# Optimization experiments

Hardware: AMD Instinct MI355X
Metric: run time of the kernel (lower is better)

## Reference

```python
import jax, jax.numpy as jnp
import numpy as np
from jax import lax

B, T, V, D, H, DH, L, INTER, K, OUT, MAXDUR, MAXLEN = 8, 128, 256, 384, 6, 64, 4, 1536, 3, 80, 8, 2048
TMEL = T * MAXDUR  # fixed padded mel length (max possible sum of durations)


def _pe(maxlen, d):
    # SinCosPositionalEncoding buffer, shape [maxlen, d]
    den = jnp.exp(-jnp.arange(0, d, 2).astype(jnp.float32) * (np.log(10000.0) / d))
    pos = jnp.arange(maxlen, dtype=jnp.float32)[:, None]
    pe = jnp.zeros((maxlen, d), jnp.float32)
    pe = pe.at[:, 0::2].set(jnp.sin(pos * den))
    pe = pe.at[:, 1::2].set(jnp.cos(pos * den))
    return pe


def _ln(x, g, b):
    m = jnp.mean(x, -1, keepdims=True)
    v = jnp.mean((x - m) ** 2, -1, keepdims=True)
    return (x - m) * lax.rsqrt(v + 1e-5) * g + b


def _conv1d(x, w, b):
    # x: [B,T,Cin], w: [K,Cin,Cout], SAME padding
    return lax.conv_general_dilated(x, w, (1,), 'SAME', dimension_numbers=('NWC', 'WIO', 'NWC')) + b


def _layer(x, mask_add, wq, wk, wv, wo, g1, b1, c1w, c1b, c2w, c2b, g2, b2):
    Bx, Tx, _ = x.shape
    q = (x @ wq).reshape(Bx, Tx, H, DH)
    k = (x @ wk).reshape(Bx, Tx, H, DH)
    v = (x @ wv).reshape(Bx, Tx, H, DH)
    s = jnp.einsum('bqhd,bkhd->bhqk', q, k) / jnp.sqrt(jnp.float32(DH))
    s = s + mask_add[:, None, None, :]  # additive -inf key mask
    a = jax.nn.softmax(s, axis=-1)
    o = jnp.einsum('bhqk,bkhd->bqhd', a, v).reshape(Bx, Tx, H * DH) @ wo
    x = _ln(x + o, g1, b1)
    h = jax.nn.relu(_conv1d(x, c1w, c1b))
    h = _conv1d(h, c2w, c2b)
    return _ln(x + h, g2, b2)


def _stack(x, mask_add, ps):
    for i in range(L):
        x = _layer(x, mask_add, *(p[i] for p in ps))
    return x


def _forward(tokens, token_lengths, durations,
             emb,
             enc_wq, enc_wk, enc_wv, enc_wo, enc_ln1g, enc_ln1b, enc_c1w, enc_c1b, enc_c2w, enc_c2b, enc_ln2g, enc_ln2b,
             dec_wq, dec_wk, dec_wv, dec_wo, dec_ln1g, dec_ln1b, dec_c1w, dec_c1b, dec_c2w, dec_c2b, dec_ln2g, dec_ln2b,
             dp_c1w, dp_c1b, dp_ln1g, dp_ln1b, dp_c2w, dp_c2b, dp_ln2g, dp_ln2b, dp_w, dp_b,
             out_w, out_b):
    x = emb[tokens]  # [B,T,D]
    pe = _pe(MAXLEN, D)
    # faithful to the torch code: pos_embedding is [maxlen,1,D] and indexed by dim-0 of a
    # batch-first tensor, so PE is indexed by BATCH index and broadcast over time; plus the
    # model adds `emb + (emb + pe)` -> 2*emb + pe.
    x = 2.0 * x + pe[:x.shape[0]][:, None, :]
    am = jnp.where(jnp.arange(T)[None, :] > token_lengths[:, None], -jnp.inf, 0.0)
    enc = _stack(x, am, (enc_wq, enc_wk, enc_wv, enc_wo, enc_ln1g, enc_ln1b,
                         enc_c1w, enc_c1b, enc_c2w, enc_c2b, enc_ln2g, enc_ln2b))
    # duration predictor: conv-relu-LN x2 + linear -> [B,T]
    h = _ln(jax.nn.relu(_conv1d(enc, dp_c1w, dp_c1b)), dp_ln1g, dp_ln1b)
    h = _ln(jax.nn.relu(_conv1d(h, dp_c2w, dp_c2b)), dp_ln2g, dp_ln2b)
    length_predictions = (h @ dp_w + dp_b)[..., 0]
    # length regulator (vectorized duplicate_by_duration, fixed TMEL padding)
    mel_len = jnp.sum(durations, axis=1)  # [B]
    cs = jnp.cumsum(durations, axis=1)    # [B,T]
    pos = jnp.arange(TMEL)
    lr = ((pos[None, None, :] < cs[:, :, None]) & (pos[None, None, :] >= (cs - durations)[:, :, None])).astype(enc.dtype)  # [B,T,TMEL]
    dec_in = jnp.einsum('btm,btd->bmd', lr, enc)  # [B,TMEL,D]
    keep = (pos[None, :] <= mel_len[:, None]).astype(dec_in.dtype)
    dec_in = dec_in * keep[:, :, None]
    am2 = jnp.where(pos[None, :] > mel_len[:, None], -jnp.inf, 0.0)
    dec = _stack(dec_in, am2, (dec_wq, dec_wk, dec_wv, dec_wo, dec_ln1g, dec_ln1b,
                               dec_c1w, dec_c1b, dec_c2w, dec_c2b, dec_ln2g, dec_ln2b))
    out = (dec @ out_w + out_b).transpose(0, 2, 1)  # [B,OUT,TMEL]
    return out, length_predictions


def setup_inputs() -> dict:
    key = jax.random.key(0)
    ks = jax.random.split(key, 64)
    cnt = [2]
    def nrm(shape):
        cnt[0] += 1
        return jax.random.normal(ks[cnt[0]], shape, jnp.float32) * 0.02
    inp = {}
    inp['tokens'] = jax.random.randint(ks[0], (B, T), 0, V)
    inp['token_lengths'] = jax.random.randint(ks[1], (B,), T // 2, T)
    inp['durations'] = jax.random.randint(ks[2], (B, T), 1, MAXDUR + 1)
    inp['emb'] = nrm((V, D))
    for pre in ('enc', 'dec'):
        inp[pre + '_wq'] = nrm((L, D, H * DH))
        inp[pre + '_wk'] = nrm((L, D, H * DH))
        inp[pre + '_wv'] = nrm((L, D, H * DH))
        inp[pre + '_wo'] = nrm((L, H * DH, D))
        inp[pre + '_ln1g'] = jnp.ones((L, D), jnp.float32)
        inp[pre + '_ln1b'] = jnp.zeros((L, D), jnp.float32)
        inp[pre + '_c1w'] = nrm((L, K, D, INTER))
        inp[pre + '_c1b'] = jnp.zeros((L, INTER), jnp.float32)
        inp[pre + '_c2w'] = nrm((L, K, INTER, D))
        inp[pre + '_c2b'] = jnp.zeros((L, D), jnp.float32)
        inp[pre + '_ln2g'] = jnp.ones((L, D), jnp.float32)
        inp[pre + '_ln2b'] = jnp.zeros((L, D), jnp.float32)
    inp['dp_c1w'] = nrm((K, D, D)); inp['dp_c1b'] = jnp.zeros((D,), jnp.float32)
    inp['dp_ln1g'] = jnp.ones((D,), jnp.float32); inp['dp_ln1b'] = jnp.zeros((D,), jnp.float32)
    inp['dp_c2w'] = nrm((K, D, D)); inp['dp_c2b'] = jnp.zeros((D,), jnp.float32)
    inp['dp_ln2g'] = jnp.ones((D,), jnp.float32); inp['dp_ln2b'] = jnp.zeros((D,), jnp.float32)
    inp['dp_w'] = nrm((D, 1)); inp['dp_b'] = jnp.zeros((1,), jnp.float32)
    inp['out_w'] = nrm((D, OUT)); inp['out_b'] = jnp.zeros((OUT,), jnp.float32)
    return inp


def reference(tokens, token_lengths, durations,
              emb,
              enc_wq, enc_wk, enc_wv, enc_wo, enc_ln1g, enc_ln1b, enc_c1w, enc_c1b, enc_c2w, enc_c2b, enc_ln2g, enc_ln2b,
              dec_wq, dec_wk, dec_wv, dec_wo, dec_ln1g, dec_ln1b, dec_c1w, dec_c1b, dec_c2w, dec_c2b, dec_ln2g, dec_ln2b,
              dp_c1w, dp_c1b, dp_ln1g, dp_ln1b, dp_c2w, dp_c2b, dp_ln2g, dp_ln2b, dp_w, dp_b,
              out_w, out_b):
    return _forward(tokens, token_lengths, durations, emb,
                    enc_wq, enc_wk, enc_wv, enc_wo, enc_ln1g, enc_ln1b, enc_c1w, enc_c1b, enc_c2w, enc_c2b, enc_ln2g, enc_ln2b,
                    dec_wq, dec_wk, dec_wv, dec_wo, dec_ln1g, dec_ln1b, dec_c1w, dec_c1b, dec_c2w, dec_c2b, dec_ln2g, dec_ln2b,
                    dp_c1w, dp_c1b, dp_ln1g, dp_ln1b, dp_c2w, dp_c2b, dp_ln2g, dp_ln2b, dp_w, dp_b,
                    out_w, out_b)
```

## Files before the change

kernel.cpp:

```cpp
#include <hip/hip_runtime.h>
#include <math.h>

typedef __bf16 bf16;
typedef __attribute__((ext_vector_type(8))) __bf16 bf16x8;
typedef __attribute__((ext_vector_type(4))) float f32x4;

constexpr int B_ = 8;
constexpr int T_ = 128;
constexpr int D_ = 384;
constexpr int H_ = 6;
constexpr int DH_ = 64;
constexpr int L_ = 4;
constexpr int INTER_ = 1536;
constexpr int OUT_C = 80;
constexpr int TMEL_ = 1024;
constexpr int HD_ = 384;
constexpr int QKV_N = 1152;

__device__ __forceinline__ int xcd_swizzle(int bid, int nwg) {
  if (nwg & 7) return bid;
  return (bid & 7) * (nwg >> 3) + (bid >> 3);
}

__global__ __launch_bounds__(256) void embed_kernel(
    const int* __restrict__ tokens, const float* __restrict__ emb,
    float* __restrict__ X, bf16* __restrict__ Xbf) {
  int i = blockIdx.x * 256 + threadIdx.x;
  if (i >= B_ * T_ * D_) return;
  int d = i % D_;
  int bt = i / D_;
  int b = bt / T_, t = bt % T_;
  int tok = tokens[bt];
  int i2 = d & ~1;
  const float c = 9.210340371976184f / (float)D_;
  float freq = expf(-(float)i2 * c);
  float ang = (float)b * freq;
  float pe = (d & 1) ? cosf(ang) : sinf(ang);
  float v = 2.0f * emb[(size_t)tok * D_ + d] + pe;
  X[i] = v;
  Xbf[((size_t)b * (T_ + 2) + 1 + t) * D_ + d] = (bf16)v;
}

__global__ void enc_mask_kernel(const int* __restrict__ tl, float* __restrict__ maske) {
  int i = blockIdx.x * 256 + threadIdx.x;
  if (i >= B_ * T_) return;
  int b = i / T_, t = i % T_;
  maske[i] = (t > tl[b]) ? -INFINITY : 0.0f;
}

__global__ __launch_bounds__(256) void transpose_w_kernel(
    const float* __restrict__ src, long srcLS, bf16* __restrict__ dst,
    long dstLS, int K, int N, int rowOfs) {
  src += (size_t)blockIdx.z * srcLS;
  dst += (size_t)blockIdx.z * dstLS;
  __shared__ float tile[32][33];
  const int tx = threadIdx.x & 31, ty = threadIdx.x >> 5;
  const int n0 = blockIdx.x * 32, k0 = blockIdx.y * 32;
#pragma unroll
  for (int j = 0; j < 4; ++j)
    tile[ty + j * 8][tx] =
        (n0 + tx < N) ? src[(size_t)(k0 + ty + j * 8) * N + n0 + tx] : 0.0f;
  __syncthreads();
#pragma unroll
  for (int j = 0; j < 4; ++j)
    dst[(size_t)(n0 + rowOfs + ty + j * 8) * K + k0 + tx] = (bf16)tile[tx][ty + j * 8];
}

__global__ void zero_pads3_kernel(bf16* a, bf16* c, bf16* m, int Tp) {
  int b = blockIdx.x >> 1, side = blockIdx.x & 1;
  size_t row = (size_t)b * (Tp + 2) + (side ? (Tp + 1) : 0);
  bf16* buf = (blockIdx.y == 0) ? a : (blockIdx.y == 1) ? c : m;
  int C = (blockIdx.y == 2) ? INTER_ : D_;
  for (int cc = threadIdx.x; cc < C; cc += 256) buf[row * C + cc] = (bf16)0.0f;
}

__global__ __launch_bounds__(256) void transpose_v_kernel(
    const bf16* __restrict__ QKV, bf16* __restrict__ VT,
    const int* __restrict__ lens, int T) {
  const int tb = blockIdx.x, db = blockIdx.y, bh = blockIdx.z;
  const int b = bh / H_, h = bh % H_;
  const int ntiles = min(T >> 6, (lens[b] + 64) >> 6);
  if (tb >= ntiles * 2) return;
  __shared__ float tile[32][33];
  const int tx = threadIdx.x & 31, ty = threadIdx.x >> 5;
  const size_t src = ((size_t)b * (T + 2) + 1 + tb * 32) * QKV_N + 768 + h * DH_ + db * 32;
#pragma unroll
  for (int j = 0; j < 4; ++j)
    tile[ty + 8 * j][tx] = (float)QKV[src + (size_t)(ty + 8 * j) * QKV_N + tx];
  __syncthreads();
  const size_t dst = ((size_t)(b * H_ + h) * DH_ + db * 32) * T + tb * 32;
#pragma unroll
  for (int j = 0; j < 4; ++j)
    VT[dst + (size_t)(ty + 8 * j) * T + tx] = (bf16)tile[tx][ty + 8 * j];
}

template <int TP>
__global__ __launch_bounds__(256) void mfma_gemm_kernel(
    const bf16* __restrict__ A, int lda, int aofs,
    const bf16* __restrict__ WT, int ldw, int kslice,
    const float* __restrict__ bias, int relu,
    float* __restrict__ Cf, float* __restrict__ Cf2,
    bf16* __restrict__ Cbf, int ldc, int transC,
    const int* __restrict__ nact) {
  __shared__ bf16 As[3][128 * 32];
  __shared__ bf16 Bs[3][128 * 32];
  const int tid = threadIdx.x;
  const int lane = tid & 63;
  const int wave = tid >> 6;
  const int wr = wave >> 1, wc = wave & 1;

  const int nT = gridDim.x, mT = gridDim.y;
  const int nwg = nT * mT * gridDim.z;
  int bid = blockIdx.x + nT * (blockIdx.y + mT * blockIdx.z);
  int wid = xcd_swizzle(bid, nwg);
  const int bx = wid % nT;
  int tmp = wid / nT;
  const int by = tmp % mT;
  const int z = tmp / mT;

  const int rowBase = by * 128;
  const int colBase = bx * 128;
  const int k0beg = z * kslice;
  const int nt = kslice / 32;
  const int bb = rowBase / TP;
  constexpr int LASTT = TP / 128 - 1;
  if (nact) {
    int tloc = (rowBase - bb * TP) >> 7;
    if (tloc >= nact[bb] && tloc != LASTT) return;
  }
  const long pr0 = (long)bb * (TP + 2) + 1 + (rowBase - bb * TP);
  const long abase = pr0 * (long)lda - aofs;

  const int srow = tid >> 2, scb = tid & 3;

  auto stage = [&](int t, int buf) {
    const int k0 = k0beg + t * 32;
#pragma unroll
    for (int e = 0; e < 2; ++e) {
      int idx = e * 256 + tid;
      int lrow = srow + e * 64;
      const bf16* gp = A + abase + (long)lrow * lda + k0 + ((scb ^ ((lrow >> 1) & 3)) << 3);
      __builtin_amdgcn_global_load_lds(
          (const __attribute__((address_space(1))) unsigned int*)gp,
          (__attribute__((address_space(3))) unsigned int*)(As[buf] + idx * 8), 16, 0, 0);
    }
#pragma unroll
    for (int e = 0; e < 2; ++e) {
      int idx = e * 256 + tid;
      int lrow = srow + e * 64;
      const bf16* gp = WT + (long)(colBase + lrow) * ldw + k0 + ((scb ^ ((lrow >> 1) & 3)) << 3);
      __builtin_amdgcn_global_load_lds(
          (const __attribute__((address_space(1))) unsigned int*)gp,
          (__attribute__((address_space(3))) unsigned int*)(Bs[buf] + idx * 8), 16, 0, 0);
    }
  };

  f32x4 acc[4][4] = {};
  const int g = lane >> 4, l15 = lane & 15;

  stage(0, 0);
  if (nt > 1) stage(1, 1);
  int cur = 0;
  for (int t = 0; t < nt; ++t) {
    if (t + 2 < nt) {
      int sb = cur + 2;
      if (sb >= 3) sb -= 3;
      stage(t + 2, sb);
    }
    int ahead = nt - 1 - t;
    if (ahead >= 2)
      asm volatile("s_waitcnt vmcnt(8)" ::: "memory");
    else if (ahead == 1)
      asm volatile("s_waitcnt vmcnt(4)" ::: "memory");
    else
      asm volatile("s_waitcnt vmcnt(0)" ::: "memory");
    __builtin_amdgcn_s_barrier();
    asm volatile("" ::: "memory");

    const bf16* Asb = As[cur];
    const bf16* Bsb = Bs[cur];
    bf16x8 af[4], bw[4];
#pragma unroll
    for (int m = 0; m < 4; ++m) {
      int row = wr * 64 + m * 16 + l15;
      int cb = g ^ ((row >> 1) & 3);
      af[m] = *(const bf16x8*)(Asb + row * 32 + cb * 8);
    }
#pragma unroll
    for (int n = 0; n < 4; ++n) {
      int row = wc * 64 + n * 16 + l15;
      int cb = g ^ ((row >> 1) & 3);
      bw[n] = *(const bf16x8*)(Bsb + row * 32 + cb * 8);
    }
#pragma unroll
    for (int m = 0; m < 4; ++m)
#pragma unroll
      for (int n = 0; n < 4; ++n)
        acc[m][n] = __builtin_amdgcn_mfma_f32_16x16x32_bf16(af[m], bw[n], acc[m][n], 0, 0, 0);

    asm volatile("" ::: "memory");
    __builtin_amdgcn_s_barrier();
    cur = (cur + 1 == 3) ? 0 : cur + 1;
  }

  float* Cfz = z ? Cf2 : Cf;
  const float* biasz = z ? nullptr : bias;
  const int qr = (lane >> 4) * 4;
  const int qc = lane & 15;
#pragma unroll
  for (int m = 0; m < 4; ++m) {
    int lrow = wr * 64 + m * 16 + qr;
#pragma unroll
    for (int n = 0; n < 4; ++n) {
      int gcol = colBase + wc * 64 + n * 16 + qc;
      float bv = (biasz && (!transC || gcol < OUT_C)) ? biasz[gcol] : 0.0f;
#pragma unroll
      for (int q = 0; q < 4; ++q) {
        float v = acc[m][n][q] + bv;
        if (relu) v = fmaxf(v, 0.0f);
        if (transC) {
          if (gcol < OUT_C)
            Cfz[((long)bb * OUT_C + gcol) * TMEL_ + (rowBase - bb * TP + lrow + q)] = v;
        } else {
          if (Cfz) Cfz[(long)(rowBase + lrow + q) * ldc + gcol] = v;
          if (Cbf) Cbf[(pr0 + lrow + q) * ldc + gcol] = (bf16)v;
        }
      }
    }
  }
}

__global__ __launch_bounds__(256) void attn4_kernel(
    const bf16* __restrict__ QKV, const bf16* __restrict__ VT,
    const float* __restrict__ maskadd, const int* __restrict__ lens,
    const int* __restrict__ nactp, bf16* __restrict__ Obf, int T) {
  const int nQT = gridDim.x;
  const int nwg = nQT * H_ * B_;
  int bid = blockIdx.x + nQT * (blockIdx.y + H_ * blockIdx.z);
  int wid = xcd_swizzle(bid, nwg);
  const int qt = wid % nQT;
  int tmp = wid / nQT;
  const int h = tmp % H_;
  const int b = tmp / H_;
  if (nactp) {
    int tloc = qt >> 1;
    if (tloc >= nactp[b] && tloc != ((T >> 7) - 1)) return;
  }

  const int tid = threadIdx.x;
  const int lane = tid & 63;
  const int wave = tid >> 6;
  const int l15 = lane & 15, g = lane >> 4;

  __shared__ bf16 Ks[64 * 64];
  __shared__ bf16 Vts[64 * 64];
  __shared__ bf16 Ps[4][16 * 64];
  __shared__ float mask_s[TMEL_];

  const int q0 = qt * 64;
  const size_t brow0 = (size_t)b * (T + 2) + 1;

  for (int i = tid; i < T; i += 256) mask_s[i] = maskadd[(size_t)b * T + i];

  const size_t qrow = brow0 + q0 + wave * 16 + l15;
  bf16x8 qf0 = *(const bf16x8*)(QKV + qrow * QKV_N + h * DH_ + g * 8);
  bf16x8 qf1 = *(const bf16x8*)(QKV + qrow * QKV_N + h * DH_ + g * 8 + 32);

  float mreg[4], lreg[4];
#pragma unroll
  for (int r = 0; r < 4; ++r) { mreg[r] = -INFINITY; lreg[r] = 0.0f; }
  f32x4 oacc[4] = {};
  bf16* Psb = Ps[wave];

  const int nt = min(T >> 6, (lens[b] + 64) >> 6);
  for (int t = 0; t < nt; ++t) {
    const int k0 = t * 64;
#pragma unroll
    for (int it = 0; it < 2; ++it) {
      int c = it * 256 + tid;
      int r = c >> 3, d0 = c & 7;
      bf16x8 kv = *(const bf16x8*)(QKV + (brow0 + k0 + r) * QKV_N + 384 + h * DH_ + d0 * 8);
      *(bf16x8*)(Ks + r * 64 + ((d0 ^ (r & 7)) << 3)) = kv;
      bf16x8 vv = *(const bf16x8*)(VT + ((size_t)(b * H_ + h) * DH_ + r) * T + k0 + d0 * 8);
      *(bf16x8*)(Vts + r * 64 + ((d0 ^ (r & 7)) << 3)) = vv;
    }
    __syncthreads();

    f32x4 sacc[4] = {};
#pragma unroll
    for (int ks = 0; ks < 2; ++ks) {
#pragma unroll
      for (int n = 0; n < 4; ++n) {
        int key = n * 16 + l15;
        bf16x8 bf = *(const bf16x8*)(Ks + key * 64 + (((g + ks * 4) ^ (key & 7)) << 3));
        sacc[n] = __builtin_amdgcn_mfma_f32_16x16x32_bf16(ks ? qf1 : qf0, bf, sacc[n], 0, 0, 0);
      }
    }

    float s[4][4];
    float tm[4] = {-INFINITY, -INFINITY, -INFINITY, -INFINITY};
#pragma unroll
    for (int n = 0; n < 4; ++n) {
      float mv = mask_s[k0 + n * 16 + l15];
#pragma unroll
      for (int r = 0; r < 4; ++r) {
        float v = sacc[n][r] * 0.125f + mv;
        s[n][r] = v;
        tm[r] = fmaxf(tm[r], v);
      }
    }
#pragma unroll
    for (int msk = 1; msk < 16; msk <<= 1)
#pragma unroll
      for (int r = 0; r < 4; ++r) tm[r] = fmaxf(tm[r], __shfl_xor(tm[r], msk));

    float sc[4];
#pragma unroll
    for (int r = 0; r < 4; ++r) {
      float mn = fmaxf(mreg[r], tm[r]);
      sc[r] = __expf(mreg[r] - mn);
      mreg[r] = mn;
    }
    float psum[4] = {0.0f, 0.0f, 0.0f, 0.0f};
#pragma unroll
    for (int n = 0; n < 4; ++n) {
      int key = n * 16 + l15;
      int kblk = key >> 3, kin = key & 7;
#pragma unroll
      for (int r = 0; r < 4; ++r) {
        float p = __expf(s[n][r] - mreg[r]);
        psum[r] += p;
        int q = g * 4 + r;
        Psb[q * 64 + ((kblk ^ (q & 7)) << 3) + kin] = (bf16)p;
      }
    }
#pragma unroll
    for (int msk = 1; msk < 16; msk <<= 1)
#pragma unroll
      for (int r = 0; r < 4; ++r) psum[r] += __shfl_xor(psum[r], msk);
#pragma unroll
    for (int r = 0; r < 4; ++r) lreg[r] = lreg[r] * sc[r] + psum[r];
#pragma unroll
    for (int n = 0; n < 4; ++n)
#pragma unroll
      for (int r = 0; r < 4; ++r) oacc[n][r] *= sc[r];

#pragma unroll
    for (int ks = 0; ks < 2; ++ks) {
      bf16x8 af = *(const bf16x8*)(Psb + l15 * 64 + (((g + ks * 4) ^ (l15 & 7)) << 3));
#pragma unroll
      for (int n = 0; n < 4; ++n) {
        int dh = n * 16 + l15;
        bf16x8 bv = *(const bf16x8*)(Vts + dh * 64 + (((g + ks * 4) ^ (dh & 7)) << 3));
        oacc[n] = __builtin_amdgcn_mfma_f32_16x16x32_bf16(af, bv, oacc[n], 0, 0, 0);
      }
    }
    __syncthreads();
  }

  float inv[4];
#pragma unroll
  for (int r = 0; r < 4; ++r) inv[r] = 1.0f / lreg[r];
  const size_t orow = brow0 + q0 + wave * 16 + g * 4;
#pragma unroll
  for (int n = 0; n < 4; ++n)
#pragma unroll
    for (int r = 0; r < 4; ++r)
      Obf[(orow + r) * D_ + h * DH_ + n * 16 + l15] = (bf16)(oacc[n][r] * inv[r]);
}

__global__ __launch_bounds__(128) void add_ln_kernel(
    const float* __restrict__ X, const float* __restrict__ H1,
    const float* __restrict__ H2,
    const float* __restrict__ g, const float* __restrict__ bb,
    float* __restrict__ Yf, bf16* __restrict__ Ybf, int tshift, int relu,
    const int* __restrict__ nactp) {
  const int row = blockIdx.x;
  const int b = row >> tshift, t = row & ((1 << tshift) - 1);
  if (nactp) {
    int tloc = t >> 7;
    if (tloc >= nactp[b] && tloc != (((1 << tshift) >> 7) - 1)) return;
  }
  const int tid = threadIdx.x;
  __shared__ float red[128];
  float v[3];
  float s = 0.0f;
#pragma unroll
  for (int e = 0; e < 3; ++e) {
    int d = tid + e * 128;
    float x = X[(size_t)row * D_ + d];
    if (H1) x += H1[(size_t)row * D_ + d];
    if (H2) x += H2[(size_t)row * D_ + d];
    if (relu) x = fmaxf(x, 0.0f);
    v[e] = x;
    s += x;
  }
  red[tid] = s;
  __syncthreads();
  for (int off = 64; off > 0; off >>= 1) {
    if (tid < off) red[tid] += red[tid + off];
    __syncthreads();
  }
  float mean = red[0] / (float)D_;
  __syncthreads();
  float s2 = 0.0f;
#pragma unroll
  for (int e = 0; e < 3; ++e) {
    float dd = v[e] - mean;
    s2 += dd * dd;
  }
  red[tid] = s2;
  __syncthreads();
  for (int off = 64; off > 0; off >>= 1) {
    if (tid < off) red[tid] += red[tid + off];
    __syncthreads();
  }
  float invstd = rsqrtf(red[0] / (float)D_ + 1e-5f);
  __syncthreads();
  const size_t prow = (size_t)b * ((1 << tshift) + 2) + 1 + t;
#pragma unroll
  for (int e = 0; e < 3; ++e) {
    int d = tid + e * 128;
    float y = (v[e] - mean) * invstd * g[d] + bb[d];
    Yf[(size_t)row * D_ + d] = y;
    if (Ybf) Ybf[prow * D_ + d] = (bf16)y;
  }
}

__global__ __launch_bounds__(64) void dp_linear_kernel(
    const float* __restrict__ Hh, const float* __restrict__ w,
    const float* __restrict__ b0, float* __restrict__ lp) {
  const int row = blockIdx.x;
  const int tid = threadIdx.x;
  float s = 0.0f;
  for (int d = tid; d < D_; d += 64) s += Hh[(size_t)row * D_ + d] * w[d];
#pragma unroll
  for (int off = 32; off > 0; off >>= 1) s += __shfl_down(s, off);
  if (tid == 0) lp[row] = s + b0[0];
}

__global__ void lr_scan_kernel(const int* __restrict__ dur, int* __restrict__ cs,
                               int* __restrict__ mel, int* __restrict__ nact) {
  int b = blockIdx.x;
  if (threadIdx.x == 0) {
    int s = 0;
    for (int t = 0; t < T_; ++t) {
      s += dur[b * T_ + t];
      cs[b * T_ + t] = s;
    }
    mel[b] = s;
    int rows = min(TMEL_, s + 9);
    nact[b] = (rows + 127) >> 7;
  }
}

__global__ __launch_bounds__(256) void lr_build_kernel(
    const int* __restrict__ cs, const int* __restrict__ mel,
    int* __restrict__ idx, float* __restrict__ maskd) {
  int b = blockIdx.x;
  int mlen = mel[b];
  for (int m = threadIdx.x; m < TMEL_; m += 256) {
    int t = -1;
    if (m < mlen) {
      int lo = 0, hi = T_ - 1;
      while (lo < hi) {
        int mid = (lo + hi) >> 1;
        if (cs[b * T_ + mid] > m) hi = mid; else lo = mid + 1;
      }
      t = lo;
    }
    idx[b * TMEL_ + m] = t;
    maskd[b * TMEL_ + m] = (m > mlen) ? -INFINITY : 0.0f;
  }
}

__global__ __launch_bounds__(128) void lr_gather_kernel(
    const float* __restrict__ XE, const int* __restrict__ idx,
    float* __restrict__ XD, bf16* __restrict__ XDbf) {
  int row = blockIdx.x;
  int b = row / TMEL_, m = row % TMEL_;
  int t = idx[row];
  size_t prow = ((size_t)b * (TMEL_ + 2) + 1 + m) * D_;
  for (int d = threadIdx.x; d < D_; d += 128) {
    float v = (t >= 0) ? XE[((size_t)(b * T_ + t)) * D_ + d] : 0.0f;
    XD[(size_t)row * D_ + d] = v;
    XDbf[prow + d] = (bf16)v;
  }
}

__global__ void halo_fix_kernel(bf16* __restrict__ buf, int C,
                                const int* __restrict__ nact) {
  int b = blockIdx.x;
  int act = nact[b] * 128;
  if (act >= 896) return;
  size_t base = (size_t)b * (TMEL_ + 2) + 1;
  size_t src = (base + act - 1) * (size_t)C;
  size_t d1 = (base + act) * (size_t)C;
  size_t d2 = (base + 895) * (size_t)C;
  for (int cc = threadIdx.x; cc < C; cc += 256) {
    bf16 v = buf[src + cc];
    buf[d1 + cc] = v;
    buf[d2 + cc] = v;
  }
}

__global__ void bcast_out_kernel(float* __restrict__ out,
                                 const int* __restrict__ nact) {
  int b = blockIdx.x / OUT_C, o = blockIdx.x % OUT_C;
  int act = nact[b] * 128;
  if (act >= 896) return;
  float* row = out + ((size_t)b * OUT_C + o) * TMEL_;
  float v = row[act - 1];
  for (int m = act + threadIdx.x; m < 896; m += 256) row[m] = v;
}

extern "C" void kernel_launch(void* const* d_in, const int* in_sizes, int n_in,
                              void* d_out, int out_size, void* d_ws, size_t ws_size,
                              hipStream_t stream) {
  const int* tokens = (const int*)d_in[0];
  const int* token_lengths = (const int*)d_in[1];
  const int* durations = (const int*)d_in[2];
  const float* emb = (const float*)d_in[3];
  const float* encw[12];
  const float* decw[12];
  for (int i = 0; i < 12; ++i) encw[i] = (const float*)d_in[4 + i];
  for (int i = 0; i < 12; ++i) decw[i] = (const float*)d_in[16 + i];
  const float* dp_c1w = (const float*)d_in[28];
  const float* dp_c1b = (const float*)d_in[29];
  const float* dp_ln1g = (const float*)d_in[30];
  const float* dp_ln1b = (const float*)d_in[31];
  const float* dp_c2w = (const float*)d_in[32];
  const float* dp_c2b = (const float*)d_in[33];
  const float* dp_ln2g = (const float*)d_in[34];
  const float* dp_ln2b = (const float*)d_in[35];
  const float* dp_w = (const float*)d_in[36];
  const float* dp_b = (const float*)d_in[37];
  const float* out_w = (const float*)d_in[38];
  const float* out_b = (const float*)d_in[39];

  float* out0 = (float*)d_out;
  float* out_lp = out0 + (size_t)B_ * OUT_C * TMEL_;

  char* wsB = (char*)d_ws;
  size_t off = 0;
  auto alloc = [&](size_t bytes) {
    void* p = wsB + off;
    off = (off + bytes + 255) & ~(size_t)255;
    return p;
  };
  float* XE = (float*)alloc((size_t)B_ * T_ * D_ * 4);
  float* XD = (float*)alloc((size_t)B_ * TMEL_ * D_ * 4);
  float* YT = (float*)alloc((size_t)B_ * TMEL_ * D_ * 4);
  bf16* XEbf = (bf16*)alloc((size_t)B_ * (T_ + 2) * D_ * 2);
  bf16* XDbf = (bf16*)alloc((size_t)B_ * (TMEL_ + 2) * D_ * 2);
  bf16* YTbf = (bf16*)alloc((size_t)B_ * (TMEL_ + 2) * D_ * 2);
  bf16* MIDbf = (bf16*)alloc((size_t)B_ * (TMEL_ + 2) * INTER_ * 2);
  bf16* QKVbf = (bf16*)alloc((size_t)B_ * (TMEL_ + 2) * QKV_N * 2);
  bf16* OBbf = (bf16*)alloc((size_t)B_ * (TMEL_ + 2) * D_ * 2);
  bf16* VTb = (bf16*)alloc((size_t)B_ * H_ * DH_ * TMEL_ * 2);
  float* OF = (float*)QKVbf;
  float* PT2 = (float*)OBbf;
  float* YTal = (float*)YT;
  bf16* QKVT = (bf16*)alloc((size_t)L_ * QKV_N * D_ * 2);
  bf16* WOT = (bf16*)alloc((size_t)L_ * D_ * D_ * 2);
  bf16* C1T = (bf16*)alloc((size_t)L_ * INTER_ * (3 * D_) * 2);
  bf16* C2T = (bf16*)alloc((size_t)L_ * D_ * (3 * INTER_) * 2);
  bf16* DP1T = (bf16*)alloc((size_t)D_ * (3 * D_) * 2);
  bf16* DP2T = (bf16*)alloc((size_t)D_ * (3 * D_) * 2);
  bf16* OUTT = (bf16*)alloc((size_t)128 * D_ * 2);
  float* MASKE = (float*)alloc(B_ * T_ * 4);
  float* MASKD = (float*)alloc(B_ * TMEL_ * 4);
  int* CS = (int*)alloc(B_ * T_ * 4);
  int* MEL = (int*)alloc(B_ * 4);
  int* NACT = (int*)alloc(B_ * 4);
  int* IDX = (int*)alloc(B_ * TMEL_ * 4);

  auto tw = [&](const float* s, long sls, bf16* d, long dls, int K, int N,
                int Ndst, int ro, int Lz) {
    transpose_w_kernel<<<dim3(Ndst / 32, K / 32, Lz), 256, 0, stream>>>(s, sls, d, dls, K, N, ro);
  };
  auto gemm = [&](int TP, int nT, int mT, int nz, const bf16* A, int lda, int aofs,
                  const bf16* WTp, int ldw, int kslice, const float* bias, int relu,
                  float* Cf, float* Cf2, bf16* Cbf, int ldc, int transC,
                  const int* nact) {
    dim3 g(nT, mT, nz);
    if (TP == 128)
      mfma_gemm_kernel<128><<<g, 256, 0, stream>>>(A, lda, aofs, WTp, ldw, kslice,
                                                   bias, relu, Cf, Cf2, Cbf, ldc, transC, nact);
    else
      mfma_gemm_kernel<1024><<<g, 256, 0, stream>>>(A, lda, aofs, WTp, ldw, kslice,
                                                    bias, relu, Cf, Cf2, Cbf, ldc, transC, nact);
  };

  auto run_layer = [&](int TP, const float* const* w, int i, float* Xf, bf16* Xbf,
                       const float* mask, const int* lens, const int* nact) {
    const int mT = B_ * TP / 128;
    const int tshift = (TP == 128) ? 7 : 10;
    gemm(TP, QKV_N / 128, mT, 1, Xbf, D_, 0, QKVT + (size_t)i * QKV_N * D_, D_, D_,
         nullptr, 0, nullptr, nullptr, QKVbf, QKV_N, 0, nact);
    transpose_v_kernel<<<dim3(TP / 32, 2, B_ * H_), 256, 0, stream>>>(QKVbf, VTb, lens, TP);
    attn4_kernel<<<dim3(TP / 64, H_, B_), 256, 0, stream>>>(QKVbf, VTb, mask, lens, nact, OBbf, TP);
    gemm(TP, D_ / 128, mT, 2, OBbf, D_, 0, WOT + (size_t)i * D_ * D_, D_, D_ / 2,
         nullptr, 0, OF, YTal, nullptr, D_, 0, nact);
    add_ln_kernel<<<B_ * TP, 128, 0, stream>>>(Xf, OF, YTal, w[4] + (size_t)i * D_,
                                               w[5] + (size_t)i * D_, YT, YTbf, tshift, 0, nact);
    if (nact) halo_fix_kernel<<<B_, 256, 0, stream>>>(YTbf, D_, nact);
    gemm(TP, INTER_ / 128, mT, 1, YTbf, D_, D_, C1T + (size_t)i * INTER_ * 3 * D_, 3 * D_,
         3 * D_, w[7] + (size_t)i * INTER_, 1, nullptr, nullptr, MIDbf, INTER_, 0, nact);
    if (nact) halo_fix_kernel<<<B_, 256, 0, stream>>>(MIDbf, INTER_, nact);
    gemm(TP, D_ / 128, mT, 2, MIDbf, INTER_, INTER_, C2T + (size_t)i * D_ * 3 * INTER_,
         3 * INTER_, 3 * INTER_ / 2, w[9] + (size_t)i * D_, 0, OF, PT2, nullptr, D_, 0, nact);
    add_ln_kernel<<<B_ * TP, 128, 0, stream>>>(YT, OF, PT2, w[10] + (size_t)i * D_,
                                               w[11] + (size_t)i * D_, Xf, Xbf, tshift, 0, nact);
  };

  embed_kernel<<<(B_ * T_ * D_ + 255) / 256, 256, 0, stream>>>(tokens, emb, XE, XEbf);
  enc_mask_kernel<<<(B_ * T_ + 255) / 256, 256, 0, stream>>>(token_lengths, MASKE);
  zero_pads3_kernel<<<dim3(B_ * 2, 3), 256, 0, stream>>>(XEbf, YTbf, MIDbf, T_);

  tw(encw[0], (long)D_ * HD_, QKVT, (long)QKV_N * D_, D_, HD_, HD_, 0, L_);
  tw(encw[1], (long)D_ * HD_, QKVT, (long)QKV_N * D_, D_, HD_, HD_, 384, L_);
  tw(encw[2], (long)D_ * HD_, QKVT, (long)QKV_N * D_, D_, HD_, HD_, 768, L_);
  tw(encw[3], (long)HD_ * D_, WOT, (long)D_ * D_, HD_, D_, D_, 0, L_);
  tw(encw[6], (long)3 * D_ * INTER_, C1T, (long)INTER_ * 3 * D_, 3 * D_, INTER_, INTER_, 0, L_);
  tw(encw[8], (long)3 * INTER_ * D_, C2T, (long)D_ * 3 * INTER_, 3 * INTER_, D_, D_, 0, L_);
  for (int i = 0; i < L_; ++i)
    run_layer(T_, encw, i, XE, XEbf, MASKE, token_lengths, nullptr);

  tw(dp_c1w, 0, DP1T, 0, 3 * D_, D_, D_, 0, 1);
  tw(dp_c2w, 0, DP2T, 0, 3 * D_, D_, D_, 0, 1);
  gemm(128, D_ / 128, B_, 2, XEbf, D_, D_, DP1T, 3 * D_, 3 * D_ / 2, dp_c1b, 0,
       OF, YTal, nullptr, D_, 0, nullptr);
  add_ln_kernel<<<B_ * T_, 128, 0, stream>>>(OF, YTal, nullptr, dp_ln1g, dp_ln1b,
                                             YT, YTbf, 7, 1, nullptr);
  gemm(128, D_ / 128, B_, 2, YTbf, D_, D_, DP2T, 3 * D_, 3 * D_ / 2, dp_c2b, 0,
       OF, YTal, nullptr, D_, 0, nullptr);
  add_ln_kernel<<<B_ * T_, 128, 0, stream>>>(OF, YTal, nullptr, dp_ln2g, dp_ln2b,
                                             YT, nullptr, 7, 1, nullptr);
  dp_linear_kernel<<<B_ * T_, 64, 0, stream>>>(YT, dp_w, dp_b, out_lp);

  lr_scan_kernel<<<B_, 32, 0, stream>>>(durations, CS, MEL, NACT);
  lr_build_kernel<<<B_, 256, 0, stream>>>(CS, MEL, IDX, MASKD);
  zero_pads3_kernel<<<dim3(B_ * 2, 3), 256, 0, stream>>>(XDbf, YTbf, MIDbf, TMEL_);
  lr_gather_kernel<<<B_ * TMEL_, 128, 0, stream>>>(XE, IDX, XD, XDbf);

  tw(decw[0], (long)D_ * HD_, QKVT, (long)QKV_N * D_, D_, HD_, HD_, 0, L_);
  tw(decw[1], (long)D_ * HD_, QKVT, (long)QKV_N * D_, D_, HD_, HD_, 384, L_);
  tw(decw[2], (long)D_ * HD_, QKVT, (long)QKV_N * D_, D_, HD_, HD_, 768, L_);
  tw(decw[3], (long)HD_ * D_, WOT, (long)D_ * D_, HD_, D_, D_, 0, L_);
  tw(decw[6], (long)3 * D_ * INTER_, C1T, (long)INTER_ * 3 * D_, 3 * D_, INTER_, INTER_, 0, L_);
  tw(decw[8], (long)3 * INTER_ * D_, C2T, (long)D_ * 3 * INTER_, 3 * INTER_, D_, D_, 0, L_);
  for (int i = 0; i < L_; ++i)
    run_layer(TMEL_, decw, i, XD, XDbf, MASKD, MEL, NACT);

  tw(out_w, 0, OUTT, 0, D_, OUT_C, 128, 0, 1);
  gemm(1024, 1, B_ * TMEL_ / 128, 1, XDbf, D_, 0, OUTT, D_, D_, out_b, 0,
       out0, nullptr, nullptr, 0, 1, NACT);
  bcast_out_kernel<<<B_ * OUT_C, 256, 0, stream>>>(out0, NACT);
}
```

Baseline: 1.389 ms.

## Fuse V transpose, halo fixes, and mask/scan kernels into producer kernels

The QKV GEMM epilogue now writes the transposed V tile directly, so the separate transpose_v kernel goes away. The halo-fix kernels are folded into the add_ln and conv1 GEMM epilogues, and the encoder mask is folded into the embed kernel. The two length-regulator kernels are merged into one that keeps the cumulative sums in shared memory, and add_ln is vectorised with float4. Together this cuts many kernel launches per layer at the cost of extra branches and scattered 4-wide V stores in the GEMM epilogue.

```diff
diff --git a/kernel.cpp b/kernel.cpp
--- a/kernel.cpp
+++ b/kernel.cpp
@@ -3,6 +3,7 @@
 
 typedef __bf16 bf16;
 typedef __attribute__((ext_vector_type(8))) __bf16 bf16x8;
+typedef __attribute__((ext_vector_type(4))) __bf16 bf16x4;
 typedef __attribute__((ext_vector_type(4))) float f32x4;
 
 constexpr int B_ = 8;
@@ -24,9 +25,14 @@
 
 __global__ __launch_bounds__(256) void embed_kernel(
     const int* __restrict__ tokens, const float* __restrict__ emb,
-    float* __restrict__ X, bf16* __restrict__ Xbf) {
+    const int* __restrict__ tl, float* __restrict__ X, bf16* __restrict__ Xbf,
+    float* __restrict__ maske) {
   int i = blockIdx.x * 256 + threadIdx.x;
   if (i >= B_ * T_ * D_) return;
+  if (i < B_ * T_) {
+    int bb = i / T_, tt = i % T_;
+    maske[i] = (tt > tl[bb]) ? -INFINITY : 0.0f;
+  }
   int d = i % D_;
   int bt = i / D_;
   int b = bt / T_, t = bt % T_;
@@ -41,13 +47,6 @@
   Xbf[((size_t)b * (T_ + 2) + 1 + t) * D_ + d] = (bf16)v;
 }
 
-__global__ void enc_mask_kernel(const int* __restrict__ tl, float* __restrict__ maske) {
-  int i = blockIdx.x * 256 + threadIdx.x;
-  if (i >= B_ * T_) return;
-  int b = i / T_, t = i % T_;
-  maske[i] = (t > tl[b]) ? -INFINITY : 0.0f;
-}
-
 __global__ __launch_bounds__(256) void transpose_w_kernel(
     const float* __restrict__ src, long srcLS, bf16* __restrict__ dst,
     long dstLS, int K, int N, int rowOfs) {
@@ -74,26 +73,6 @@
   for (int cc = threadIdx.x; cc < C; cc += 256) buf[row * C + cc] = (bf16)0.0f;
 }
 
-__global__ __launch_bounds__(256) void transpose_v_kernel(
-    const bf16* __restrict__ QKV, bf16* __restrict__ VT,
-    const int* __restrict__ lens, int T) {
-  const int tb = blockIdx.x, db = blockIdx.y, bh = blockIdx.z;
-  const int b = bh / H_, h = bh % H_;
-  const int ntiles = min(T >> 6, (lens[b] + 64) >> 6);
-  if (tb >= ntiles * 2) return;
-  __shared__ float tile[32][33];
-  const int tx = threadIdx.x & 31, ty = threadIdx.x >> 5;
-  const size_t src = ((size_t)b * (T + 2) + 1 + tb * 32) * QKV_N + 768 + h * DH_ + db * 32;
-#pragma unroll
-  for (int j = 0; j < 4; ++j)
-    tile[ty + 8 * j][tx] = (float)QKV[src + (size_t)(ty + 8 * j) * QKV_N + tx];
-  __syncthreads();
-  const size_t dst = ((size_t)(b * H_ + h) * DH_ + db * 32) * T + tb * 32;
-#pragma unroll
-  for (int j = 0; j < 4; ++j)
-    VT[dst + (size_t)(ty + 8 * j) * T + tx] = (bf16)tile[tx][ty + 8 * j];
-}
-
 template <int TP>
 __global__ __launch_bounds__(256) void mfma_gemm_kernel(
     const bf16* __restrict__ A, int lda, int aofs,
@@ -101,7 +80,7 @@
     const float* __restrict__ bias, int relu,
     float* __restrict__ Cf, float* __restrict__ Cf2,
     bf16* __restrict__ Cbf, int ldc, int transC,
-    const int* __restrict__ nact) {
+    const int* __restrict__ nact, bf16* __restrict__ VTout, int haloC) {
   __shared__ bf16 As[3][128 * 32];
   __shared__ bf16 Bs[3][128 * 32];
   const int tid = threadIdx.x;
@@ -207,23 +186,53 @@
   const float* biasz = z ? nullptr : bias;
   const int qr = (lane >> 4) * 4;
   const int qc = lane & 15;
+  const int actR = (haloC && nact) ? nact[bb] * 128 : -1;
 #pragma unroll
   for (int m = 0; m < 4; ++m) {
     int lrow = wr * 64 + m * 16 + qr;
+    int tl0 = rowBase - bb * TP + lrow;
 #pragma unroll
     for (int n = 0; n < 4; ++n) {
       int gcol = colBase + wc * 64 + n * 16 + qc;
       float bv = (biasz && (!transC || gcol < OUT_C)) ? biasz[gcol] : 0.0f;
+      float vq[4];
 #pragma unroll
       for (int q = 0; q < 4; ++q) {
         float v = acc[m][n][q] + bv;
         if (relu) v = fmaxf(v, 0.0f);
-        if (transC) {
-          if (gcol < OUT_C)
-            Cfz[((long)bb * OUT_C + gcol) * TMEL_ + (rowBase - bb * TP + lrow + q)] = v;
-        } else {
-          if (Cfz) Cfz[(long)(rowBase + lrow + q) * ldc + gcol] = v;
-          if (Cbf) Cbf[(pr0 + lrow + q) * ldc + gcol] = (bf16)v;
+        vq[q] = v;
+      }
+      if (transC) {
+        if (gcol < OUT_C)
+#pragma unroll
+          for (int q = 0; q < 4; ++q)
+            Cfz[((long)bb * OUT_C + gcol) * TMEL_ + tl0 + q] = vq[q];
+      } else {
+        if (Cfz)
+#pragma unroll
+          for (int q = 0; q < 4; ++q)
+            Cfz[(long)(rowBase + lrow + q) * ldc + gcol] = vq[q];
+        if (Cbf) {
+#pragma unroll
+          for (int q = 0; q < 4; ++q)
+            Cbf[(pr0 + lrow + q) * ldc + gcol] = (bf16)vq[q];
+          if (actR >= 0 && actR < 896) {
+#pragma unroll
+            for (int q = 0; q < 4; ++q)
+              if (tl0 + q == actR - 1) {
+                long pb = (long)bb * (TP + 2) + 1;
+                bf16 hv = (bf16)vq[q];
+                Cbf[(pb + actR) * (long)ldc + gcol] = hv;
+                Cbf[(pb + 895) * (long)ldc + gcol] = hv;
+              }
+          }
+        }
+        if (VTout && gcol >= 768) {
+          int hh = (gcol - 768) >> 6, dh = (gcol - 768) & 63;
+          bf16x4 pk;
+#pragma unroll
+          for (int q = 0; q < 4; ++q) pk[q] = (bf16)vq[q];
+          *(bf16x4*)(VTout + (((size_t)(bb * H_ + hh) * DH_ + dh) * TP + tl0)) = pk;
         }
       }
     }
@@ -374,7 +383,7 @@
     const float* __restrict__ H2,
     const float* __restrict__ g, const float* __restrict__ bb,
     float* __restrict__ Yf, bf16* __restrict__ Ybf, int tshift, int relu,
-    const int* __restrict__ nactp) {
+    const int* __restrict__ nactp, int halo) {
   const int row = blockIdx.x;
   const int b = row >> tshift, t = row & ((1 << tshift) - 1);
   if (nactp) {
@@ -382,20 +391,25 @@
     if (tloc >= nactp[b] && tloc != (((1 << tshift) >> 7) - 1)) return;
   }
   const int tid = threadIdx.x;
+  const bool lact = tid < 96;
   __shared__ float red[128];
-  float v[3];
-  float s = 0.0f;
-#pragma unroll
-  for (int e = 0; e < 3; ++e) {
-    int d = tid + e * 128;
-    float x = X[(size_t)row * D_ + d];
-    if (H1) x += H1[(size_t)row * D_ + d];
-    if (H2) x += H2[(size_t)row * D_ + d];
-    if (relu) x = fmaxf(x, 0.0f);
-    v[e] = x;
-    s += x;
-  }
-  red[tid] = s;
+  float4 v = make_float4(0.f, 0.f, 0.f, 0.f);
+  if (lact) {
+    v = ((const float4*)(X + (size_t)row * D_))[tid];
+    if (H1) {
+      float4 h = ((const float4*)(H1 + (size_t)row * D_))[tid];
+      v.x += h.x; v.y += h.y; v.z += h.z; v.w += h.w;
+    }
+    if (H2) {
+      float4 h = ((const float4*)(H2 + (size_t)row * D_))[tid];
+      v.x += h.x; v.y += h.y; v.z += h.z; v.w += h.w;
+    }
+    if (relu) {
+      v.x = fmaxf(v.x, 0.f); v.y = fmaxf(v.y, 0.f);
+      v.z = fmaxf(v.z, 0.f); v.w = fmaxf(v.w, 0.f);
+    }
+  }
+  red[tid] = v.x + v.y + v.z + v.w;
   __syncthreads();
   for (int off = 64; off > 0; off >>= 1) {
     if (tid < off) red[tid] += red[tid + off];
@@ -403,13 +417,8 @@
   }
   float mean = red[0] / (float)D_;
   __syncthreads();
-  float s2 = 0.0f;
-#pragma unroll
-  for (int e = 0; e < 3; ++e) {
-    float dd = v[e] - mean;
-    s2 += dd * dd;
-  }
-  red[tid] = s2;
+  float dx = v.x - mean, dy = v.y - mean, dz = v.z - mean, dw = v.w - mean;
+  red[tid] = lact ? (dx * dx + dy * dy + dz * dz + dw * dw) : 0.0f;
   __syncthreads();
   for (int off = 64; off > 0; off >>= 1) {
     if (tid < off) red[tid] += red[tid + off];
@@ -417,13 +426,27 @@
   }
   float invstd = rsqrtf(red[0] / (float)D_ + 1e-5f);
   __syncthreads();
-  const size_t prow = (size_t)b * ((1 << tshift) + 2) + 1 + t;
-#pragma unroll
-  for (int e = 0; e < 3; ++e) {
-    int d = tid + e * 128;
-    float y = (v[e] - mean) * invstd * g[d] + bb[d];
-    Yf[(size_t)row * D_ + d] = y;
-    if (Ybf) Ybf[prow * D_ + d] = (bf16)y;
+  if (!lact) return;
+  float4 gv = ((const float4*)g)[tid];
+  float4 bv = ((const float4*)bb)[tid];
+  float4 y;
+  y.x = dx * invstd * gv.x + bv.x;
+  y.y = dy * invstd * gv.y + bv.y;
+  y.z = dz * invstd * gv.z + bv.z;
+  y.w = dw * invstd * gv.w + bv.w;
+  ((float4*)(Yf + (size_t)row * D_))[tid] = y;
+  if (Ybf) {
+    const size_t pbase = (size_t)b * ((1 << tshift) + 2) + 1;
+    bf16x4 p;
+    p[0] = (bf16)y.x; p[1] = (bf16)y.y; p[2] = (bf16)y.z; p[3] = (bf16)y.w;
+    *(bf16x4*)(Ybf + (pbase + t) * D_ + tid * 4) = p;
+    if (halo && nactp) {
+      int act = nactp[b] * 128;
+      if (act < 896 && t == act - 1) {
+        *(bf16x4*)(Ybf + (pbase + act) * D_ + tid * 4) = p;
+        *(bf16x4*)(Ybf + (pbase + 895) * D_ + tid * 4) = p;
+      }
+    }
   }
 }
 
@@ -439,33 +462,31 @@
   if (tid == 0) lp[row] = s + b0[0];
 }
 
-__global__ void lr_scan_kernel(const int* __restrict__ dur, int* __restrict__ cs,
-                               int* __restrict__ mel, int* __restrict__ nact) {
+__global__ __launch_bounds__(256) void lr_prep_kernel(
+    const int* __restrict__ dur, int* __restrict__ mel, int* __restrict__ nact,
+    int* __restrict__ idx, float* __restrict__ maskd) {
   int b = blockIdx.x;
+  __shared__ int cs_s[T_];
+  __shared__ int smel;
   if (threadIdx.x == 0) {
     int s = 0;
     for (int t = 0; t < T_; ++t) {
       s += dur[b * T_ + t];
-      cs[b * T_ + t] = s;
-    }
+      cs_s[t] = s;
+    }
+    smel = s;
     mel[b] = s;
-    int rows = min(TMEL_, s + 9);
-    nact[b] = (rows + 127) >> 7;
-  }
-}
-
-__global__ __launch_bounds__(256) void lr_build_kernel(
-    const int* __restrict__ cs, const int* __restrict__ mel,
-    int* __restrict__ idx, float* __restrict__ maskd) {
-  int b = blockIdx.x;
-  int mlen = mel[b];
+    nact[b] = (min(TMEL_, s + 9) + 127) >> 7;
+  }
+  __syncthreads();
+  int mlen = smel;
   for (int m = threadIdx.x; m < TMEL_; m += 256) {
     int t = -1;
     if (m < mlen) {
       int lo = 0, hi = T_ - 1;
       while (lo < hi) {
         int mid = (lo + hi) >> 1;
-        if (cs[b * T_ + mid] > m) hi = mid; else lo = mid + 1;
+        if (cs_s[mid] > m) hi = mid; else lo = mid + 1;
       }
       t = lo;
     }
@@ -485,22 +506,6 @@
     float v = (t >= 0) ? XE[((size_t)(b * T_ + t)) * D_ + d] : 0.0f;
     XD[(size_t)row * D_ + d] = v;
     XDbf[prow + d] = (bf16)v;
-  }
-}
-
-__global__ void halo_fix_kernel(bf16* __restrict__ buf, int C,
-                                const int* __restrict__ nact) {
-  int b = blockIdx.x;
-  int act = nact[b] * 128;
-  if (act >= 896) return;
-  size_t base = (size_t)b * (TMEL_ + 2) + 1;
-  size_t src = (base + act - 1) * (size_t)C;
-  size_t d1 = (base + act) * (size_t)C;
-  size_t d2 = (base + 895) * (size_t)C;
-  for (int cc = threadIdx.x; cc < C; cc += 256) {
-    bf16 v = buf[src + cc];
-    buf[d1 + cc] = v;
-    buf[d2 + cc] = v;
   }
 }
 
@@ -570,7 +575,6 @@
   bf16* OUTT = (bf16*)alloc((size_t)128 * D_ * 2);
   float* MASKE = (float*)alloc(B_ * T_ * 4);
   float* MASKD = (float*)alloc(B_ * TMEL_ * 4);
-  int* CS = (int*)alloc(B_ * T_ * 4);
   int* MEL = (int*)alloc(B_ * 4);
   int* NACT = (int*)alloc(B_ * 4);
   int* IDX = (int*)alloc(B_ * TMEL_ * 4);
@@ -582,14 +586,16 @@
   auto gemm = [&](int TP, int nT, int mT, int nz, const bf16* A, int lda, int aofs,
                   const bf16* WTp, int ldw, int kslice, const float* bias, int relu,
                   float* Cf, float* Cf2, bf16* Cbf, int ldc, int transC,
-                  const int* nact) {
+                  const int* nact, bf16* VTout, int haloC) {
     dim3 g(nT, mT, nz);
     if (TP == 128)
       mfma_gemm_kernel<128><<<g, 256, 0, stream>>>(A, lda, aofs, WTp, ldw, kslice,
-                                                   bias, relu, Cf, Cf2, Cbf, ldc, transC, nact);
+                                                   bias, relu, Cf, Cf2, Cbf, ldc, transC,
+                                                   nact, VTout, haloC);
     else
       mfma_gemm_kernel<1024><<<g, 256, 0, stream>>>(A, lda, aofs, WTp, ldw, kslice,
-                                                    bias, relu, Cf, Cf2, Cbf, ldc, transC, nact);
+                                                    bias, relu, Cf, Cf2, Cbf, ldc, transC,
+                                                    nact, VTout, haloC);
   };
 
   auto run_layer = [&](int TP, const float* const* w, int i, float* Xf, bf16* Xbf,
@@ -597,25 +603,26 @@
     const int mT = B_ * TP / 128;
     const int tshift = (TP == 128) ? 7 : 10;
     gemm(TP, QKV_N / 128, mT, 1, Xbf, D_, 0, QKVT + (size_t)i * QKV_N * D_, D_, D_,
-         nullptr, 0, nullptr, nullptr, QKVbf, QKV_N, 0, nact);
-    transpose_v_kernel<<<dim3(TP / 32, 2, B_ * H_), 256, 0, stream>>>(QKVbf, VTb, lens, TP);
+         nullptr, 0, nullptr, nullptr, QKVbf, QKV_N, 0, nact, VTb, 0);
     attn4_kernel<<<dim3(TP / 64, H_, B_), 256, 0, stream>>>(QKVbf, VTb, mask, lens, nact, OBbf, TP);
     gemm(TP, D_ / 128, mT, 2, OBbf, D_, 0, WOT + (size_t)i * D_ * D_, D_, D_ / 2,
-         nullptr, 0, OF, YTal, nullptr, D_, 0, nact);
+         nullptr, 0, OF, YTal, nullptr, D_, 0, nact, nullptr, 0);
     add_ln_kernel<<<B_ * TP, 128, 0, stream>>>(Xf, OF, YTal, w[4] + (size_t)i * D_,
-                                               w[5] + (size_t)i * D_, YT, YTbf, tshift, 0, nact);
-    if (nact) halo_fix_kernel<<<B_, 256, 0, stream>>>(YTbf, D_, nact);
+                                               w[5] + (size_t)i * D_, YT, YTbf, tshift, 0,
+                                               nact, 1);
     gemm(TP, INTER_ / 128, mT, 1, YTbf, D_, D_, C1T + (size_t)i * INTER_ * 3 * D_, 3 * D_,
-         3 * D_, w[7] + (size_t)i * INTER_, 1, nullptr, nullptr, MIDbf, INTER_, 0, nact);
-    if (nact) halo_fix_kernel<<<B_, 256, 0, stream>>>(MIDbf, INTER_, nact);
+         3 * D_, w[7] + (size_t)i * INTER_, 1, nullptr, nullptr, MIDbf, INTER_, 0,
+         nact, nullptr, 1);
     gemm(TP, D_ / 128, mT, 2, MIDbf, INTER_, INTER_, C2T + (size_t)i * D_ * 3 * INTER_,
-         3 * INTER_, 3 * INTER_ / 2, w[9] + (size_t)i * D_, 0, OF, PT2, nullptr, D_, 0, nact);
+         3 * INTER_, 3 * INTER_ / 2, w[9] + (size_t)i * D_, 0, OF, PT2, nullptr, D_, 0,
+         nact, nullptr, 0);
     add_ln_kernel<<<B_ * TP, 128, 0, stream>>>(YT, OF, PT2, w[10] + (size_t)i * D_,
-                                               w[11] + (size_t)i * D_, Xf, Xbf, tshift, 0, nact);
+                                               w[11] + (size_t)i * D_, Xf, Xbf, tshift, 0,
+                                               nact, 0);
   };
 
-  embed_kernel<<<(B_ * T_ * D_ + 255) / 256, 256, 0, stream>>>(tokens, emb, XE, XEbf);
-  enc_mask_kernel<<<(B_ * T_ + 255) / 256, 256, 0, stream>>>(token_lengths, MASKE);
+  embed_kernel<<<(B_ * T_ * D_ + 255) / 256, 256, 0, stream>>>(tokens, emb, token_lengths,
+                                                               XE, XEbf, MASKE);
   zero_pads3_kernel<<<dim3(B_ * 2, 3), 256, 0, stream>>>(XEbf, YTbf, MIDbf, T_);
 
   tw(encw[0], (long)D_ * HD_, QKVT, (long)QKV_N * D_, D_, HD_, HD_, 0, L_);
@@ -630,17 +637,16 @@
   tw(dp_c1w, 0, DP1T, 0, 3 * D_, D_, D_, 0, 1);
   tw(dp_c2w, 0, DP2T, 0, 3 * D_, D_, D_, 0, 1);
   gemm(128, D_ / 128, B_, 2, XEbf, D_, D_, DP1T, 3 * D_, 3 * D_ / 2, dp_c1b, 0,
-       OF, YTal, nullptr, D_, 0, nullptr);
+       OF, YTal, nullptr, D_, 0, nullptr, nullptr, 0);
   add_ln_kernel<<<B_ * T_, 128, 0, stream>>>(OF, YTal, nullptr, dp_ln1g, dp_ln1b,
-                                             YT, YTbf, 7, 1, nullptr);
+                                             YT, YTbf, 7, 1, nullptr, 0);
   gemm(128, D_ / 128, B_, 2, YTbf, D_, D_, DP2T, 3 * D_, 3 * D_ / 2, dp_c2b, 0,
-       OF, YTal, nullptr, D_, 0, nullptr);
+       OF, YTal, nullptr, D_, 0, nullptr, nullptr, 0);
   add_ln_kernel<<<B_ * T_, 128, 0, stream>>>(OF, YTal, nullptr, dp_ln2g, dp_ln2b,
-                                             YT, nullptr, 7, 1, nullptr);
+                                             YT, nullptr, 7, 1, nullptr, 0);
   dp_linear_kernel<<<B_ * T_, 64, 0, stream>>>(YT, dp_w, dp_b, out_lp);
 
-  lr_scan_kernel<<<B_, 32, 0, stream>>>(durations, CS, MEL, NACT);
-  lr_build_kernel<<<B_, 256, 0, stream>>>(CS, MEL, IDX, MASKD);
+  lr_prep_kernel<<<B_, 256, 0, stream>>>(durations, MEL, NACT, IDX, MASKD);
   zero_pads3_kernel<<<dim3(B_ * 2, 3), 256, 0, stream>>>(XDbf, YTbf, MIDbf, TMEL_);
   lr_gather_kernel<<<B_ * TMEL_, 128, 0, stream>>>(XE, IDX, XD, XDbf);
 
@@ -655,6 +661,6 @@
 
   tw(out_w, 0, OUTT, 0, D_, OUT_C, 128, 0, 1);
   gemm(1024, 1, B_ * TMEL_ / 128, 1, XDbf, D_, 0, OUTT, D_, D_, out_b, 0,
-       out0, nullptr, nullptr, 0, 1, NACT);
+       out0, nullptr, nullptr, 0, 1, NACT, nullptr, 0);
   bcast_out_kernel<<<B_ * OUT_C, 256, 0, stream>>>(out0, NACT);
 }
```

Result: faster. 1.276 ms (-8.2%).
